# Optimization experiments

Measured on AMD Instinct MI355X. Metric: run time of the kernel, lower is better.

## Reference

```python
import jax, jax.numpy as jnp
import numpy as np

P = 1024   # total patches = B * n_patches
B = 32
NPATCH = 32
D = 64
EPS = 1e-6


def _mlp2(x, W1, b1, W2, b2):
    # Linear -> ReLU -> (Dropout p=0) -> Linear
    return jax.nn.relu(x @ W1 + b1) @ W2 + b2


def setup_inputs() -> dict:
    key = jax.random.key(0)
    ks = jax.random.split(key, 32)
    d = D
    inp = {}
    inp['x'] = jax.random.normal(ks[0], (65536, d), dtype=jnp.float32)
    inp['subgraphs_nodes_mapper'] = jax.random.randint(ks[1], (65536,), 0, 65536)
    inp['subgraphs_batch'] = jnp.sort(jax.random.randint(ks[2], (65536,), 0, P))
    inp['subgraphs_batch_row'] = jax.random.randint(ks[3], (16384,), 0, P)
    inp['subgraphs_batch_col'] = jax.random.randint(ks[4], (16384,), 0, P)
    inp['coarsen_edge_attr'] = jax.random.uniform(ks[5], (16384,), dtype=jnp.float32)
    s = 1.0 / np.sqrt(d)
    def W(k, shape):
        return jax.random.normal(k, shape, dtype=jnp.float32) * s
    # input_transform (Linear,ReLU,Linear,ReLU)
    inp['Wt1'] = W(ks[6], (d, d)); inp['bt1'] = jnp.zeros((d,), jnp.float32)
    inp['Wt2'] = W(ks[7], (d, d)); inp['bt2'] = jnp.zeros((d,), jnp.float32)
    # pre / post deepset (2 layers each)
    inp['Wpre1'] = W(ks[8], (d, d)); inp['bpre1'] = jnp.zeros((d,), jnp.float32)
    inp['Wpre2'] = W(ks[9], (d, d)); inp['bpre2'] = jnp.zeros((d,), jnp.float32)
    inp['Wpost1'] = W(ks[10], (d, d)); inp['bpost1'] = jnp.zeros((d,), jnp.float32)
    inp['Wpost2'] = W(ks[11], (d, d)); inp['bpost2'] = jnp.zeros((d,), jnp.float32)
    # linK / linV
    inp['Wk'] = W(ks[12], (d, d)); inp['bk'] = jnp.zeros((d,), jnp.float32)
    inp['Wv'] = W(ks[13], (d, d)); inp['bv'] = jnp.zeros((d,), jnp.float32)
    # attention-based readout seed
    inp['seed'] = jax.random.normal(ks[14], (d,), dtype=jnp.float32)
    # classifier: Linear(d, d//2), ReLU, Linear(d//2, num_classes)
    inp['Wc1'] = W(ks[15], (d, d // 2)); inp['bc1'] = jnp.zeros((d // 2,), jnp.float32)
    inp['Wc2'] = W(ks[16], (d // 2, 10)); inp['bc2'] = jnp.zeros((10,), jnp.float32)
    return inp


def reference(x, subgraphs_nodes_mapper, subgraphs_batch, subgraphs_batch_row,
              subgraphs_batch_col, coarsen_edge_attr,
              Wt1, bt1, Wt2, bt2,
              Wpre1, bpre1, Wpre2, bpre2,
              Wpost1, bpost1, Wpost2, bpost2,
              Wk, bk, Wv, bv, seed,
              Wc1, bc1, Wc2, bc2):
    seg = jax.ops.segment_sum
    row, col, batch = subgraphs_batch_row, subgraphs_batch_col, subgraphs_batch

    # input_transform then gather onto subgraph-combined node set
    h = jax.nn.relu(jax.nn.relu(x @ Wt1 + bt1) @ Wt2 + bt2)
    hs = h[subgraphs_nodes_mapper]                        # [N, d]

    # symmetric random-walk normalization of coarsened edge weights
    deg = seg(coarsen_edge_attr, row, num_segments=P)
    dinv = jnp.where(deg > 0, jax.lax.rsqrt(jnp.maximum(deg, EPS)), 0.0)
    attr = dinv[row] * coarsen_edge_attr * dinv[col]      # [E]

    # Q: pre-deepset -> scatter-sum per patch -> post-deepset
    Q = _mlp2(hs, Wpre1, bpre1, Wpre2, bpre2)
    Qs = seg(Q, batch, num_segments=P)                    # [P, d]
    Qs = _mlp2(Qs, Wpost1, bpost1, Wpost2, bpost2)

    # K: linear proj, scatter-mean per patch; V: linear proj (node level)
    K = hs @ Wk + bk
    cnt = seg(jnp.ones_like(K[:, 0]), batch, num_segments=P)
    Ks = seg(K, batch, num_segments=P) / jnp.maximum(cnt, 1.0)[:, None]
    V = hs @ Wv + bv

    # relu kernel feature maps
    Qk = jax.nn.relu(Qs)                                  # [P, d]
    Kk = jax.nn.relu(K)                                   # [N, d]
    Ksk = jax.nn.relu(Ks)                                 # [P, d]

    # linear attention state per patch: M_p = sum_{i in p} k_i v_i^T
    M = seg(Kk[:, :, None] * V[:, None, :], batch, num_segments=P)  # [P, d, d]
    # random-walk message / key propagation on coarsened patch graph
    M = M + seg(attr[:, None, None] * M[col], row, num_segments=P)
    Kagg = Ksk + seg(attr[:, None] * Ksk[col], row, num_segments=P)

    # kernelized attention readout per patch
    num = jnp.einsum('pd,pde->pe', Qk, M)
    den = jnp.sum(Qk * Kagg, axis=-1)
    out = num / (den[:, None] + EPS)                      # [P, d]

    # (B p) d -> B p d, attention-based set readout with learned seed
    out = out.reshape(B, NPATCH, D)
    scores = jax.nn.softmax((out @ seed) / jnp.sqrt(jnp.float32(D)), axis=1)
    pooled = jnp.einsum('bp,bpd->bd', scores, out)        # [B, d]

    # classifier
    logits = jax.nn.relu(pooled @ Wc1 + bc1) @ Wc2 + bc2  # [B, num_classes]
    return logits
```

## Files before the change

### kernel.cpp

```cpp
#include <hip/hip_runtime.h>
#include <cstddef>

#define NND  65536
#define PP   1024
#define EE   16384
#define TJA  48
#define TI   32
#define EPSF 1e-6f

typedef unsigned int   u32;
typedef unsigned short u16;
typedef __attribute__((ext_vector_type(8))) short bf16x8;
typedef __attribute__((ext_vector_type(4))) float f32x4;

__device__ __forceinline__ u16 f2bf(float f) {
    u32 u = __float_as_uint(f);
    u += 0x7fffu + ((u >> 16) & 1u);
    return (u16)(u >> 16);
}
__device__ __forceinline__ float bflo(u32 u) { return __uint_as_float(u << 16); }
__device__ __forceinline__ float bfhi(u32 u) { return __uint_as_float(u & 0xffff0000u); }
__device__ __forceinline__ float bf1(u16 v)  { return __uint_as_float(((u32)v) << 16); }


__global__ void patch_bounds_kernel(const int* __restrict__ batch, int* __restrict__ start) {
    int i = blockIdx.x * blockDim.x + threadIdx.x;
    if (i >= NND) return;
    int b  = batch[i];
    int bp = (i == 0) ? -1 : batch[i - 1];
    for (int p = bp + 1; p <= b; ++p) start[p] = i;
    if (i == NND - 1) {
        for (int p = b + 1; p <= PP; ++p) start[p] = NND;
    }
}

__global__ void edge_hist_kernel(const int* __restrict__ row, const int* __restrict__ col,
                                 const float* __restrict__ attr,
                                 float* __restrict__ deg, int* __restrict__ colcnt) {
    int e = blockIdx.x * blockDim.x + threadIdx.x;
    if (e >= EE) return;
    atomicAdd(&deg[row[e]], attr[e]);
    atomicAdd(&colcnt[col[e]], 1);
}

__global__ void scan_dinv_kernel(const int* __restrict__ colcnt, int* __restrict__ col_start,
                                 const float* __restrict__ deg, float* __restrict__ dinv) {
    __shared__ int s[PP];
    int t = threadIdx.x;
    s[t] = colcnt[t];
    float dg = deg[t];
    dinv[t] = (dg > 0.f) ? rsqrtf(fmaxf(dg, EPSF)) : 0.f;
    __syncthreads();
    for (int off = 1; off < PP; off <<= 1) {
        int v = (t >= off) ? s[t - off] : 0;
        __syncthreads();
        s[t] += v;
        __syncthreads();
    }
    col_start[t + 1] = s[t];
    if (t == 0) col_start[0] = 0;
}

__global__ void edge_scatter_kernel(const int* __restrict__ col, const int* __restrict__ col_start,
                                    int* __restrict__ colfill, int* __restrict__ edge_perm) {
    int e = blockIdx.x * blockDim.x + threadIdx.x;
    if (e >= EE) return;
    int c = col[e];
    int pos = col_start[c] + atomicAdd(&colfill[c], 1);
    edge_perm[pos] = e;
}

__global__ __launch_bounds__(256)
void pack_w_kernel(const float* W0, const float* W1, const float* W2, const float* W3,
                   const float* W4, const float* W5, const float* W6, const float* W7,
                   u16* __restrict__ out) {
    const float* Ws[8] = {W0, W1, W2, W3, W4, W5, W6, W7};
    const float* W = Ws[blockIdx.x];
    u16* dst = out + (size_t)blockIdx.x * 4096;
    int t = threadIdx.x;
    for (int idx = t; idx < 512; idx += 256) {
        int f = idx >> 6, l = idx & 63;
        int kk = f >> 2, nt = f & 3;
        int g = l >> 4, m = l & 15;
#pragma unroll
        for (int j = 0; j < 8; ++j) {
            int k = kk * 32 + g * 8 + j;
            int n = nt * 16 + m;
            dst[idx * 8 + j] = f2bf(W[k * 64 + n]);
        }
    }
}


__device__ __forceinline__ void stage_f32(const float* __restrict__ in, u16* s, int row0, int t) {
    int r = t >> 2, c = t & 3;
    const float4* src = (const float4*)(in + (size_t)(row0 + r) * 64 + c * 16);
    char* sb = (char*)s + r * 128;
    int swz = (r & 7) << 4;
#pragma unroll
    for (int q4 = 0; q4 < 4; ++q4) {
        float4 v = src[q4];
        u32 p0 = (u32)f2bf(v.x) | ((u32)f2bf(v.y) << 16);
        u32 p1 = (u32)f2bf(v.z) | ((u32)f2bf(v.w) << 16);
        int pc = c * 8 + q4 * 2;
        *(u32*)(sb + ((pc * 4) ^ swz))       = p0;
        *(u32*)(sb + (((pc + 1) * 4) ^ swz)) = p1;
    }
}

__device__ __forceinline__ void stage_bf16_gather(const u16* __restrict__ h,
                                                  const int* __restrict__ gmap,
                                                  u16* s, int row0, int t) {
    int r = t >> 2, c = t & 3;
    int sr = gmap[row0 + r];
    const uint4* src = (const uint4*)(h + (size_t)sr * 64) + c * 2;
    uint4 a = src[0], b = src[1];
    char* sb = (char*)s + r * 128;
    int swz = (r & 7) << 4;
    *(uint4*)(sb + ((c * 32) ^ swz))      = a;
    *(uint4*)(sb + ((c * 32 + 16) ^ swz)) = b;
}

template <bool RELU>
__device__ __forceinline__ void gemm_layer(const u16* src, u16* dst,
                                           const u16* __restrict__ Wp,
                                           const float* __restrict__ bias,
                                           int wv, int lane) {
    int g = lane >> 4, m = lane & 15;
    int arow = wv * 16 + m;
    const char* sb = (const char*)src + arow * 128;
    int aswz = (arow & 7) << 4;
    bf16x8 a0 = *(const bf16x8*)(sb + ((g * 16) ^ aswz));
    bf16x8 a1 = *(const bf16x8*)(sb + ((64 + g * 16) ^ aswz));
    const bf16x8* wp = (const bf16x8*)Wp;
#pragma unroll
    for (int ntile = 0; ntile < 4; ++ntile) {
        float bv = bias[ntile * 16 + m];
        f32x4 acc = {bv, bv, bv, bv};
        acc = __builtin_amdgcn_mfma_f32_16x16x32_bf16(a0, wp[(0 * 4 + ntile) * 64 + lane], acc, 0, 0, 0);
        acc = __builtin_amdgcn_mfma_f32_16x16x32_bf16(a1, wp[(1 * 4 + ntile) * 64 + lane], acc, 0, 0, 0);
        int col = ntile * 16 + m;
#pragma unroll
        for (int rg = 0; rg < 4; ++rg) {
            float v = acc[rg];
            if (RELU) v = fmaxf(v, 0.f);
            int rr = wv * 16 + g * 4 + rg;
            *(u16*)((char*)dst + rr * 128 + ((2 * col) ^ ((rr & 7) << 4))) = f2bf(v);
        }
    }
}

template <bool RELU>
__device__ __forceinline__ void gemm_layer_f32out(const u16* src, float* __restrict__ out,
                                                  const u16* __restrict__ Wp,
                                                  const float* __restrict__ bias,
                                                  int row0, int wv, int lane) {
    int g = lane >> 4, m = lane & 15;
    int arow = wv * 16 + m;
    const char* sb = (const char*)src + arow * 128;
    int aswz = (arow & 7) << 4;
    bf16x8 a0 = *(const bf16x8*)(sb + ((g * 16) ^ aswz));
    bf16x8 a1 = *(const bf16x8*)(sb + ((64 + g * 16) ^ aswz));
    const bf16x8* wp = (const bf16x8*)Wp;
#pragma unroll
    for (int ntile = 0; ntile < 4; ++ntile) {
        float bv = bias[ntile * 16 + m];
        f32x4 acc = {bv, bv, bv, bv};
        acc = __builtin_amdgcn_mfma_f32_16x16x32_bf16(a0, wp[(0 * 4 + ntile) * 64 + lane], acc, 0, 0, 0);
        acc = __builtin_amdgcn_mfma_f32_16x16x32_bf16(a1, wp[(1 * 4 + ntile) * 64 + lane], acc, 0, 0, 0);
        int col = ntile * 16 + m;
#pragma unroll
        for (int rg = 0; rg < 4; ++rg) {
            float v = acc[rg];
            if (RELU) v = fmaxf(v, 0.f);
            out[(size_t)(row0 + wv * 16 + g * 4 + rg) * 64 + col] = v;
        }
    }
}

__device__ __forceinline__ void copy_out_bf16(const u16* s, u16* __restrict__ g, int row0, int t) {
    int r = t >> 2, c = t & 3;
    const char* sb = (const char*)s + r * 128;
    int swz = (r & 7) << 4;
    uint4 a = *(const uint4*)(sb + ((c * 32) ^ swz));
    uint4 b = *(const uint4*)(sb + ((c * 32 + 16) ^ swz));
    uint4* dst = (uint4*)(g + (size_t)(row0 + r) * 64) + c * 2;
    dst[0] = a; dst[1] = b;
}

template <bool OUT_BF16>
__global__ __launch_bounds__(256)
void mfma_mlp2_kernel(const float* __restrict__ in,
                      const u16* __restrict__ Wp1, const float* __restrict__ b1,
                      const u16* __restrict__ Wp2, const float* __restrict__ b2,
                      void* __restrict__ out) {
    __shared__ __align__(16) u16 xs[4096];
    __shared__ __align__(16) u16 ys[4096];
    int t = threadIdx.x, lane = t & 63, wv = t >> 6;
    int row0 = blockIdx.x * 64;
    stage_f32(in, xs, row0, t);
    gemm_layer<true>(xs, ys, Wp1, b1, wv, lane);
    if (OUT_BF16) {
        gemm_layer<true>(ys, xs, Wp2, b2, wv, lane);
        copy_out_bf16(xs, (u16*)out, row0, t);
    } else {
        gemm_layer_f32out<true>(ys, (float*)out, Wp2, b2, row0, wv, lane);
    }
}

__global__ __launch_bounds__(256)
void qkv_mfma_kernel(const u16* __restrict__ h, const int* __restrict__ gmap,
                     const u16* __restrict__ Wpk, const float* __restrict__ bk,
                     const u16* __restrict__ Wpv, const float* __restrict__ bv,
                     const u16* __restrict__ Wp1, const float* __restrict__ bp1,
                     const u16* __restrict__ Wp2, const float* __restrict__ bp2,
                     u16* __restrict__ Kout, u16* __restrict__ Vout, u16* __restrict__ Qout) {
    __shared__ __align__(16) u16 xs[4096];
    __shared__ __align__(16) u16 ys[4096];
    int t = threadIdx.x, lane = t & 63, wv = t >> 6;
    int row0 = blockIdx.x * 64;
    stage_bf16_gather(h, gmap, xs, row0, t);
    gemm_layer<false>(xs, ys, Wpk, bk, wv, lane);
    copy_out_bf16(ys, Kout, row0, t);
    gemm_layer<false>(xs, ys, Wpv, bv, wv, lane);
    copy_out_bf16(ys, Vout, row0, t);
    gemm_layer<true>(xs, ys, Wp1, bp1, wv, lane);
    gemm_layer<false>(ys, xs, Wp2, bp2, wv, lane);
    copy_out_bf16(xs, Qout, row0, t);
}

__global__ __launch_bounds__(256)
void patch_reduce_kernel(const u16* __restrict__ Qn, const u16* __restrict__ K,
                         const int* __restrict__ start,
                         float* __restrict__ Qs_raw, float* __restrict__ Ksk) {
    __shared__ float qred[4][64], kred[4][64];
    int p = blockIdx.x, t = threadIdx.x;
    int d = t & 63, s = t >> 6;
    int i0 = start[p], i1 = start[p + 1];
    float qa = 0.f, ka = 0.f;
    for (int i = i0 + s; i < i1; i += 4) {
        qa += bf1(Qn[(size_t)i * 64 + d]);
        ka += bf1(K[(size_t)i * 64 + d]);
    }
    qred[s][d] = qa; kred[s][d] = ka;
    __syncthreads();
    if (s == 0) {
        float q = qred[0][d] + qred[1][d] + qred[2][d] + qred[3][d];
        float k = kred[0][d] + kred[1][d] + kred[2][d] + kred[3][d];
        Qs_raw[(size_t)p * 64 + d] = q;
        int cnt = i1 - i0;
        Ksk[(size_t)p * 64 + d] = fmaxf(k / (float)max(cnt, 1), 0.f);
    }
}

__global__ __launch_bounds__(256)
void attn_kernel(const float* __restrict__ Qk, const u16* __restrict__ K,
                 const u16* __restrict__ V, const float* __restrict__ Ksk,
                 const int* __restrict__ e_row, const float* __restrict__ e_attr,
                 const int* __restrict__ edge_perm, const int* __restrict__ col_start,
                 const int* __restrict__ patch_start, const float* __restrict__ dinv,
                 float* __restrict__ num, float* __restrict__ Kagg) {
    __shared__ float Qs[TJA][65];
    __shared__ float accN[TJA][65];
    __shared__ float Ks_[TI][65];
    __shared__ float Vs[TI][65];
    __shared__ float dots[TJA][TI];
    __shared__ float coef[TJA];
    __shared__ int   trow[TJA];
    __shared__ float Ksc[64];
    int c = blockIdx.x, t = threadIdx.x;
    int e0 = col_start[c], e1 = col_start[c + 1];
    int ntgt = e1 - e0 + 1;
    int i0 = patch_start[c], i1 = patch_start[c + 1];
    float dc = dinv[c];
    if (t < 64) Ksc[t] = Ksk[(size_t)c * 64 + t];

    for (int jc = 0; jc < ntgt; jc += TJA) {
        int mj = min(TJA, ntgt - jc);
        __syncthreads();
        if (t < mj) {
            int j = jc + t; int p; float cf;
            if (j == 0) { p = c; cf = 1.f; }
            else { int e = edge_perm[e0 + j - 1]; p = e_row[e]; cf = dinv[p] * e_attr[e] * dc; }
            trow[t] = p; coef[t] = cf;
        }
        __syncthreads();
        for (int idx = t; idx < mj * 64; idx += 256) {
            int j = idx >> 6, d = idx & 63;
            Qs[j][d] = Qk[(size_t)trow[j] * 64 + d];
            accN[j][d] = 0.f;
        }
        __syncthreads();
        for (int ic = i0; ic < i1; ic += TI) {
            int ni = min(TI, i1 - ic);
            for (int idx = t; idx < ni * 16; idx += 256) {
                int i = idx >> 4, q = idx & 15;
                uint2 kv = ((const uint2*)(K + (size_t)(ic + i) * 64))[q];
                uint2 vv = ((const uint2*)(V + (size_t)(ic + i) * 64))[q];
                float* kd = &Ks_[i][q * 4];
                kd[0] = fmaxf(bflo(kv.x), 0.f); kd[1] = fmaxf(bfhi(kv.x), 0.f);
                kd[2] = fmaxf(bflo(kv.y), 0.f); kd[3] = fmaxf(bfhi(kv.y), 0.f);
                float* vd = &Vs[i][q * 4];
                vd[0] = bflo(vv.x); vd[1] = bfhi(vv.x);
                vd[2] = bflo(vv.y); vd[3] = bfhi(vv.y);
            }
            __syncthreads();
            for (int idx = t; idx < mj * TI; idx += 256) {
                int j = idx >> 5, i = idx & (TI - 1);
                float s = 0.f;
#pragma unroll
                for (int d = 0; d < 64; ++d) s = fmaf(Qs[j][d], Ks_[i][d], s);
                dots[j][i] = s;
            }
            __syncthreads();
            {
                int d0 = (t & 15) * 4;
                for (int j = t >> 4; j < mj; j += 16) {
                    float a0 = accN[j][d0],     a1 = accN[j][d0 + 1];
                    float a2 = accN[j][d0 + 2], a3 = accN[j][d0 + 3];
                    for (int i = 0; i < ni; ++i) {
                        float dv = dots[j][i];
                        a0 = fmaf(dv, Vs[i][d0],     a0);
                        a1 = fmaf(dv, Vs[i][d0 + 1], a1);
                        a2 = fmaf(dv, Vs[i][d0 + 2], a2);
                        a3 = fmaf(dv, Vs[i][d0 + 3], a3);
                    }
                    accN[j][d0] = a0; accN[j][d0 + 1] = a1;
                    accN[j][d0 + 2] = a2; accN[j][d0 + 3] = a3;
                }
            }
            __syncthreads();
        }
        for (int idx = t; idx < mj * 64; idx += 256) {
            int j = idx >> 6, d = idx & 63;
            float cf = coef[j];
            atomicAdd(&num[(size_t)trow[j] * 64 + d],  cf * accN[j][d]);
            atomicAdd(&Kagg[(size_t)trow[j] * 64 + d], cf * Ksc[d]);
        }
    }
}

__global__ __launch_bounds__(64)
void final_kernel(const float* __restrict__ num, const float* __restrict__ Qk,
                  const float* __restrict__ Kagg, const float* __restrict__ seed,
                  const float* __restrict__ Wc1, const float* __restrict__ bc1,
                  const float* __restrict__ Wc2, const float* __restrict__ bc2,
                  float* __restrict__ logits) {
    __shared__ float s_out[32][65];
    __shared__ float s_rd[32], s_sc[32], s_pool[64], s_c1[32], s_seed[64];
    int b = blockIdx.x, t = threadIdx.x;
    s_seed[t] = seed[t];
    if (t < 32) {
        int p = b * 32 + t;
        float den = 0.f;
        for (int d = 0; d < 64; ++d)
            den = fmaf(Qk[(size_t)p * 64 + d], Kagg[(size_t)p * 64 + d], den);
        s_rd[t] = 1.f / (den + EPSF);
    }
    __syncthreads();
    for (int p = 0; p < 32; ++p)
        s_out[p][t] = num[(size_t)(b * 32 + p) * 64 + t] * s_rd[p];
    __syncthreads();
    if (t < 32) {
        float sc = 0.f;
        for (int d = 0; d < 64; ++d) sc = fmaf(s_out[t][d], s_seed[d], sc);
        s_sc[t] = sc * 0.125f;
    }
    __syncthreads();
    if (t == 0) {
        float mx = -1e30f;
        for (int p = 0; p < 32; ++p) mx = fmaxf(mx, s_sc[p]);
        float sm = 0.f;
        for (int p = 0; p < 32; ++p) { float e = expf(s_sc[p] - mx); s_sc[p] = e; sm += e; }
        float inv = 1.f / sm;
        for (int p = 0; p < 32; ++p) s_sc[p] *= inv;
    }
    __syncthreads();
    {
        float pa = 0.f;
        for (int p = 0; p < 32; ++p) pa = fmaf(s_sc[p], s_out[p][t], pa);
        s_pool[t] = pa;
    }
    __syncthreads();
    if (t < 32) {
        float a = bc1[t];
        for (int d = 0; d < 64; ++d) a = fmaf(s_pool[d], Wc1[d * 32 + t], a);
        s_c1[t] = fmaxf(a, 0.f);
    }
    __syncthreads();
    if (t < 10) {
        float a = bc2[t];
        for (int j = 0; j < 32; ++j) a = fmaf(s_c1[j], Wc2[j * 10 + t], a);
        logits[b * 10 + t] = a;
    }
}


extern "C" void kernel_launch(void* const* d_in, const int* in_sizes, int n_in,
                              void* d_out, int out_size, void* d_ws, size_t ws_size,
                              hipStream_t stream) {
    const float* x      = (const float*)d_in[0];
    const int*   mapper = (const int*)d_in[1];
    const int*   batch  = (const int*)d_in[2];
    const int*   e_row  = (const int*)d_in[3];
    const int*   e_col  = (const int*)d_in[4];
    const float* e_attr = (const float*)d_in[5];
    const float* Wt1 = (const float*)d_in[6],  *bt1 = (const float*)d_in[7];
    const float* Wt2 = (const float*)d_in[8],  *bt2 = (const float*)d_in[9];
    const float* Wpre1 = (const float*)d_in[10], *bpre1 = (const float*)d_in[11];
    const float* Wpre2 = (const float*)d_in[12], *bpre2 = (const float*)d_in[13];
    const float* Wpost1 = (const float*)d_in[14], *bpost1 = (const float*)d_in[15];
    const float* Wpost2 = (const float*)d_in[16], *bpost2 = (const float*)d_in[17];
    const float* Wk = (const float*)d_in[18], *bk = (const float*)d_in[19];
    const float* Wv = (const float*)d_in[20], *bv = (const float*)d_in[21];
    const float* seed = (const float*)d_in[22];
    const float* Wc1 = (const float*)d_in[23], *bc1 = (const float*)d_in[24];
    const float* Wc2 = (const float*)d_in[25], *bc2 = (const float*)d_in[26];
    float* logits = (float*)d_out;

    char* w = (char*)d_ws;
    const size_t NB2 = (size_t)NND * 64 * 2;
    u16* hb  = (u16*)w;             w += NB2;
    u16* Kb  = (u16*)w;             w += NB2;
    u16* Vb  = (u16*)w;             w += NB2;
    u16* Qnb = (u16*)w;             w += NB2;
    u16* Wp  = (u16*)w;             w += 8 * 4096 * 2;
    float* numb   = (float*)w;      w += PP * 64 * 4;
    float* Kagg   = (float*)w;      w += PP * 64 * 4;
    float* Qs_raw = (float*)w;      w += PP * 64 * 4;
    float* Qkb    = (float*)w;      w += PP * 64 * 4;
    float* Kskb   = (float*)w;      w += PP * 64 * 4;
    float* deg    = (float*)w;      w += PP * 4;
    int*   colcnt = (int*)w;        w += PP * 4;
    int*   colfill= (int*)w;        w += PP * 4;
    float* dinv   = (float*)w;      w += PP * 4;
    int* patch_start = (int*)w;     w += (PP + 1) * 4;
    int* col_start   = (int*)w;     w += (PP + 1) * 4;
    int* edge_perm   = (int*)w;     w += EE * 4;

    hipMemsetAsync(numb, 0, 2 * PP * 64 * sizeof(float), stream);
    hipMemsetAsync(deg, 0, 3 * PP * sizeof(int), stream);

    patch_bounds_kernel<<<NND / 256, 256, 0, stream>>>(batch, patch_start);
    edge_hist_kernel<<<EE / 256, 256, 0, stream>>>(e_row, e_col, e_attr, deg, colcnt);
    scan_dinv_kernel<<<1, PP, 0, stream>>>(colcnt, col_start, deg, dinv);
    edge_scatter_kernel<<<EE / 256, 256, 0, stream>>>(e_col, col_start, colfill, edge_perm);

    pack_w_kernel<<<8, 256, 0, stream>>>(Wt1, Wt2, Wk, Wv, Wpre1, Wpre2, Wpost1, Wpost2, Wp);

    mfma_mlp2_kernel<true><<<NND / 64, 256, 0, stream>>>(
        x, Wp + 0 * 4096, bt1, Wp + 1 * 4096, bt2, hb);
    qkv_mfma_kernel<<<NND / 64, 256, 0, stream>>>(
        hb, mapper, Wp + 2 * 4096, bk, Wp + 3 * 4096, bv,
        Wp + 4 * 4096, bpre1, Wp + 5 * 4096, bpre2, Kb, Vb, Qnb);
    patch_reduce_kernel<<<PP, 256, 0, stream>>>(Qnb, Kb, patch_start, Qs_raw, Kskb);
    mfma_mlp2_kernel<false><<<PP / 64, 256, 0, stream>>>(
        Qs_raw, Wp + 6 * 4096, bpost1, Wp + 7 * 4096, bpost2, Qkb);
    attn_kernel<<<PP, 256, 0, stream>>>(Qkb, Kb, Vb, Kskb, e_row, e_attr, edge_perm,
                                        col_start, patch_start, dinv, numb, Kagg);
    final_kernel<<<32, 64, 0, stream>>>(numb, Qkb, Kagg, seed, Wc1, bc1, Wc2, bc2, logits);
}
```

Baseline: 214.9 us.

## Rewrite attention kernel with bf16 shared tiles and per-wave dot/accumulate

Replaces the attention kernel with a version that keeps K, V and Q tiles in shared memory as bf16, with relu applied via a packed bit mask. It uses larger node chunks (88) and a per-wave row loop that computes dots and then accumulates V into a shared accumulator. Qk is now stored as bf16, so the post-MLP kernel uses the bf16 output path. The patch reduction reads packed u32 pairs with 8 row slices. This cuts shared memory footprint and global traffic, but lowers Qk precision and serializes target rows across only 4 waves.

```diff
diff --git a/kernel.cpp b/kernel.cpp
--- a/kernel.cpp
+++ b/kernel.cpp
@@ -4,8 +4,8 @@
 #define NND  65536
 #define PP   1024
 #define EE   16384
-#define TJA  48
-#define TI   32
+#define CAP  88
+#define TJ2  32
 #define EPSF 1e-6f
 
 typedef unsigned int   u32;
@@ -21,6 +21,10 @@
 __device__ __forceinline__ float bflo(u32 u) { return __uint_as_float(u << 16); }
 __device__ __forceinline__ float bfhi(u32 u) { return __uint_as_float(u & 0xffff0000u); }
 __device__ __forceinline__ float bf1(u16 v)  { return __uint_as_float(((u32)v) << 16); }
+__device__ __forceinline__ u32 relu2(u32 v) {
+    u32 mask = ((v & 0x80008000u) >> 15) * 0xFFFFu;
+    return v & ~mask;
+}
 
 
 __global__ void patch_bounds_kernel(const int* __restrict__ batch, int* __restrict__ start) {
@@ -150,34 +154,6 @@
     }
 }
 
-template <bool RELU>
-__device__ __forceinline__ void gemm_layer_f32out(const u16* src, float* __restrict__ out,
-                                                  const u16* __restrict__ Wp,
-                                                  const float* __restrict__ bias,
-                                                  int row0, int wv, int lane) {
-    int g = lane >> 4, m = lane & 15;
-    int arow = wv * 16 + m;
-    const char* sb = (const char*)src + arow * 128;
-    int aswz = (arow & 7) << 4;
-    bf16x8 a0 = *(const bf16x8*)(sb + ((g * 16) ^ aswz));
-    bf16x8 a1 = *(const bf16x8*)(sb + ((64 + g * 16) ^ aswz));
-    const bf16x8* wp = (const bf16x8*)Wp;
-#pragma unroll
-    for (int ntile = 0; ntile < 4; ++ntile) {
-        float bv = bias[ntile * 16 + m];
-        f32x4 acc = {bv, bv, bv, bv};
-        acc = __builtin_amdgcn_mfma_f32_16x16x32_bf16(a0, wp[(0 * 4 + ntile) * 64 + lane], acc, 0, 0, 0);
-        acc = __builtin_amdgcn_mfma_f32_16x16x32_bf16(a1, wp[(1 * 4 + ntile) * 64 + lane], acc, 0, 0, 0);
-        int col = ntile * 16 + m;
-#pragma unroll
-        for (int rg = 0; rg < 4; ++rg) {
-            float v = acc[rg];
-            if (RELU) v = fmaxf(v, 0.f);
-            out[(size_t)(row0 + wv * 16 + g * 4 + rg) * 64 + col] = v;
-        }
-    }
-}
-
 __device__ __forceinline__ void copy_out_bf16(const u16* s, u16* __restrict__ g, int row0, int t) {
     int r = t >> 2, c = t & 3;
     const char* sb = (const char*)s + r * 128;
@@ -188,24 +164,19 @@
     dst[0] = a; dst[1] = b;
 }
 
-template <bool OUT_BF16>
 __global__ __launch_bounds__(256)
 void mfma_mlp2_kernel(const float* __restrict__ in,
                       const u16* __restrict__ Wp1, const float* __restrict__ b1,
                       const u16* __restrict__ Wp2, const float* __restrict__ b2,
-                      void* __restrict__ out) {
+                      u16* __restrict__ out) {
     __shared__ __align__(16) u16 xs[4096];
     __shared__ __align__(16) u16 ys[4096];
     int t = threadIdx.x, lane = t & 63, wv = t >> 6;
     int row0 = blockIdx.x * 64;
     stage_f32(in, xs, row0, t);
     gemm_layer<true>(xs, ys, Wp1, b1, wv, lane);
-    if (OUT_BF16) {
-        gemm_layer<true>(ys, xs, Wp2, b2, wv, lane);
-        copy_out_bf16(xs, (u16*)out, row0, t);
-    } else {
-        gemm_layer_f32out<true>(ys, (float*)out, Wp2, b2, row0, wv, lane);
-    }
+    gemm_layer<true>(ys, xs, Wp2, b2, wv, lane);
+    copy_out_bf16(xs, out, row0, t);
 }
 
 __global__ __launch_bounds__(256)
@@ -233,115 +204,117 @@
 void patch_reduce_kernel(const u16* __restrict__ Qn, const u16* __restrict__ K,
                          const int* __restrict__ start,
                          float* __restrict__ Qs_raw, float* __restrict__ Ksk) {
-    __shared__ float qred[4][64], kred[4][64];
+    __shared__ float qred[8][64], kred[8][64];
     int p = blockIdx.x, t = threadIdx.x;
-    int d = t & 63, s = t >> 6;
+    int w = t & 31, s = t >> 5;
     int i0 = start[p], i1 = start[p + 1];
-    float qa = 0.f, ka = 0.f;
-    for (int i = i0 + s; i < i1; i += 4) {
-        qa += bf1(Qn[(size_t)i * 64 + d]);
-        ka += bf1(K[(size_t)i * 64 + d]);
-    }
-    qred[s][d] = qa; kred[s][d] = ka;
-    __syncthreads();
-    if (s == 0) {
-        float q = qred[0][d] + qred[1][d] + qred[2][d] + qred[3][d];
-        float k = kred[0][d] + kred[1][d] + kred[2][d] + kred[3][d];
-        Qs_raw[(size_t)p * 64 + d] = q;
+    float qa0 = 0.f, qa1 = 0.f, ka0 = 0.f, ka1 = 0.f;
+    for (int i = i0 + s; i < i1; i += 8) {
+        u32 qv = ((const u32*)(Qn + (size_t)i * 64))[w];
+        u32 kv = ((const u32*)(K  + (size_t)i * 64))[w];
+        qa0 += bflo(qv); qa1 += bfhi(qv);
+        ka0 += bflo(kv); ka1 += bfhi(kv);
+    }
+    qred[s][w * 2] = qa0; qred[s][w * 2 + 1] = qa1;
+    kred[s][w * 2] = ka0; kred[s][w * 2 + 1] = ka1;
+    __syncthreads();
+    if (t < 64) {
+        float q = 0.f, k = 0.f;
+#pragma unroll
+        for (int z = 0; z < 8; ++z) { q += qred[z][t]; k += kred[z][t]; }
+        Qs_raw[(size_t)p * 64 + t] = q;
         int cnt = i1 - i0;
-        Ksk[(size_t)p * 64 + d] = fmaxf(k / (float)max(cnt, 1), 0.f);
+        Ksk[(size_t)p * 64 + t] = fmaxf(k / (float)max(cnt, 1), 0.f);
     }
 }
 
 __global__ __launch_bounds__(256)
-void attn_kernel(const float* __restrict__ Qk, const u16* __restrict__ K,
-                 const u16* __restrict__ V, const float* __restrict__ Ksk,
-                 const int* __restrict__ e_row, const float* __restrict__ e_attr,
-                 const int* __restrict__ edge_perm, const int* __restrict__ col_start,
-                 const int* __restrict__ patch_start, const float* __restrict__ dinv,
-                 float* __restrict__ num, float* __restrict__ Kagg) {
-    __shared__ float Qs[TJA][65];
-    __shared__ float accN[TJA][65];
-    __shared__ float Ks_[TI][65];
-    __shared__ float Vs[TI][65];
-    __shared__ float dots[TJA][TI];
-    __shared__ float coef[TJA];
-    __shared__ int   trow[TJA];
+void attn2_kernel(const u16* __restrict__ Qkb, const u16* __restrict__ Kb,
+                  const u16* __restrict__ Vb, const float* __restrict__ Kskb,
+                  const int* __restrict__ e_row, const float* __restrict__ e_attr,
+                  const int* __restrict__ edge_perm, const int* __restrict__ col_start,
+                  const int* __restrict__ patch_start, const float* __restrict__ dinv,
+                  float* __restrict__ num, float* __restrict__ Kagg) {
+    __shared__ u16   Ks[CAP * 66];
+    __shared__ u16   Vs[CAP * 66];
+    __shared__ u16   Qs[TJ2 * 66];
+    __shared__ float accS[TJ2 * 64];
+    __shared__ float dots[4][CAP];
+    __shared__ float coef[TJ2];
+    __shared__ int   trow[TJ2];
     __shared__ float Ksc[64];
-    int c = blockIdx.x, t = threadIdx.x;
+    int c = blockIdx.x, t = threadIdx.x, wv = t >> 6, lane = t & 63;
     int e0 = col_start[c], e1 = col_start[c + 1];
     int ntgt = e1 - e0 + 1;
     int i0 = patch_start[c], i1 = patch_start[c + 1];
     float dc = dinv[c];
-    if (t < 64) Ksc[t] = Ksk[(size_t)c * 64 + t];
-
-    for (int jc = 0; jc < ntgt; jc += TJA) {
-        int mj = min(TJA, ntgt - jc);
+    if (t < 64) Ksc[t] = Kskb[(size_t)c * 64 + t];
+
+    for (int tc = 0; tc < ntgt; tc += TJ2) {
+        int mj = min(TJ2, ntgt - tc);
         __syncthreads();
         if (t < mj) {
-            int j = jc + t; int p; float cf;
+            int j = tc + t; int p; float cf;
             if (j == 0) { p = c; cf = 1.f; }
             else { int e = edge_perm[e0 + j - 1]; p = e_row[e]; cf = dinv[p] * e_attr[e] * dc; }
             trow[t] = p; coef[t] = cf;
         }
+        for (int idx = t; idx < mj * 64; idx += 256) accS[idx] = 0.f;
+        __syncthreads();
+        for (int idx = t; idx < mj * 32; idx += 256) {
+            int j = idx >> 5, q = idx & 31;
+            u32 v = ((const u32*)(Qkb + (size_t)trow[j] * 64))[q];
+            *(u32*)&Qs[j * 66 + q * 2] = v;
+        }
+        for (int ic = i0; ic < i1; ic += CAP) {
+            int nc = min(CAP, i1 - ic);
+            __syncthreads();
+            for (int idx = t; idx < nc * 8; idx += 256) {
+                int i = idx >> 3, q = idx & 7;
+                uint4 kv = *((const uint4*)(Kb + (size_t)(ic + i) * 64) + q);
+                uint4 vv = *((const uint4*)(Vb + (size_t)(ic + i) * 64) + q);
+                u32* kd = (u32*)&Ks[i * 66 + q * 8];
+                kd[0] = relu2(kv.x); kd[1] = relu2(kv.y);
+                kd[2] = relu2(kv.z); kd[3] = relu2(kv.w);
+                u32* vd = (u32*)&Vs[i * 66 + q * 8];
+                vd[0] = vv.x; vd[1] = vv.y; vd[2] = vv.z; vd[3] = vv.w;
+            }
+            __syncthreads();
+            for (int j = wv; j < mj; j += 4) {
+                for (int ib = 0; ib < nc; ib += 64) {
+                    int i = ib + lane;
+                    if (i < nc) {
+                        float dot = 0.f;
+                        const u32* kr = (const u32*)&Ks[i * 66];
+                        const u32* qr = (const u32*)&Qs[j * 66];
+#pragma unroll 8
+                        for (int q = 0; q < 32; ++q) {
+                            u32 kw = kr[q], qw = qr[q];
+                            dot = fmaf(bflo(qw), bflo(kw), dot);
+                            dot = fmaf(bfhi(qw), bfhi(kw), dot);
+                        }
+                        dots[wv][i] = dot;
+                    }
+                }
+                float out = 0.f;
+#pragma unroll 4
+                for (int i = 0; i < nc; ++i)
+                    out = fmaf(dots[wv][i], bf1(Vs[i * 66 + lane]), out);
+                accS[j * 64 + lane] += out;
+            }
+        }
         __syncthreads();
         for (int idx = t; idx < mj * 64; idx += 256) {
             int j = idx >> 6, d = idx & 63;
-            Qs[j][d] = Qk[(size_t)trow[j] * 64 + d];
-            accN[j][d] = 0.f;
-        }
-        __syncthreads();
-        for (int ic = i0; ic < i1; ic += TI) {
-            int ni = min(TI, i1 - ic);
-            for (int idx = t; idx < ni * 16; idx += 256) {
-                int i = idx >> 4, q = idx & 15;
-                uint2 kv = ((const uint2*)(K + (size_t)(ic + i) * 64))[q];
-                uint2 vv = ((const uint2*)(V + (size_t)(ic + i) * 64))[q];
-                float* kd = &Ks_[i][q * 4];
-                kd[0] = fmaxf(bflo(kv.x), 0.f); kd[1] = fmaxf(bfhi(kv.x), 0.f);
-                kd[2] = fmaxf(bflo(kv.y), 0.f); kd[3] = fmaxf(bfhi(kv.y), 0.f);
-                float* vd = &Vs[i][q * 4];
-                vd[0] = bflo(vv.x); vd[1] = bfhi(vv.x);
-                vd[2] = bflo(vv.y); vd[3] = bfhi(vv.y);
-            }
-            __syncthreads();
-            for (int idx = t; idx < mj * TI; idx += 256) {
-                int j = idx >> 5, i = idx & (TI - 1);
-                float s = 0.f;
-#pragma unroll
-                for (int d = 0; d < 64; ++d) s = fmaf(Qs[j][d], Ks_[i][d], s);
-                dots[j][i] = s;
-            }
-            __syncthreads();
-            {
-                int d0 = (t & 15) * 4;
-                for (int j = t >> 4; j < mj; j += 16) {
-                    float a0 = accN[j][d0],     a1 = accN[j][d0 + 1];
-                    float a2 = accN[j][d0 + 2], a3 = accN[j][d0 + 3];
-                    for (int i = 0; i < ni; ++i) {
-                        float dv = dots[j][i];
-                        a0 = fmaf(dv, Vs[i][d0],     a0);
-                        a1 = fmaf(dv, Vs[i][d0 + 1], a1);
-                        a2 = fmaf(dv, Vs[i][d0 + 2], a2);
-                        a3 = fmaf(dv, Vs[i][d0 + 3], a3);
-                    }
-                    accN[j][d0] = a0; accN[j][d0 + 1] = a1;
-                    accN[j][d0 + 2] = a2; accN[j][d0 + 3] = a3;
-                }
-            }
-            __syncthreads();
-        }
-        for (int idx = t; idx < mj * 64; idx += 256) {
-            int j = idx >> 6, d = idx & 63;
             float cf = coef[j];
-            atomicAdd(&num[(size_t)trow[j] * 64 + d],  cf * accN[j][d]);
+            atomicAdd(&num[(size_t)trow[j] * 64 + d],  cf * accS[j * 64 + d]);
             atomicAdd(&Kagg[(size_t)trow[j] * 64 + d], cf * Ksc[d]);
         }
     }
 }
 
 __global__ __launch_bounds__(64)
-void final_kernel(const float* __restrict__ num, const float* __restrict__ Qk,
+void final_kernel(const float* __restrict__ num, const u16* __restrict__ Qk,
                   const float* __restrict__ Kagg, const float* __restrict__ seed,
                   const float* __restrict__ Wc1, const float* __restrict__ bc1,
                   const float* __restrict__ Wc2, const float* __restrict__ bc2,
@@ -354,7 +327,7 @@
         int p = b * 32 + t;
         float den = 0.f;
         for (int d = 0; d < 64; ++d)
-            den = fmaf(Qk[(size_t)p * 64 + d], Kagg[(size_t)p * 64 + d], den);
+            den = fmaf(bf1(Qk[(size_t)p * 64 + d]), Kagg[(size_t)p * 64 + d], den);
         s_rd[t] = 1.f / (den + EPSF);
     }
     __syncthreads();
@@ -425,10 +398,10 @@
     u16* Vb  = (u16*)w;             w += NB2;
     u16* Qnb = (u16*)w;             w += NB2;
     u16* Wp  = (u16*)w;             w += 8 * 4096 * 2;
+    u16* Qkb = (u16*)w;             w += PP * 64 * 2;
     float* numb   = (float*)w;      w += PP * 64 * 4;
     float* Kagg   = (float*)w;      w += PP * 64 * 4;
     float* Qs_raw = (float*)w;      w += PP * 64 * 4;
-    float* Qkb    = (float*)w;      w += PP * 64 * 4;
     float* Kskb   = (float*)w;      w += PP * 64 * 4;
     float* deg    = (float*)w;      w += PP * 4;
     int*   colcnt = (int*)w;        w += PP * 4;
@@ -448,15 +421,15 @@
 
     pack_w_kernel<<<8, 256, 0, stream>>>(Wt1, Wt2, Wk, Wv, Wpre1, Wpre2, Wpost1, Wpost2, Wp);
 
-    mfma_mlp2_kernel<true><<<NND / 64, 256, 0, stream>>>(
+    mfma_mlp2_kernel<<<NND / 64, 256, 0, stream>>>(
         x, Wp + 0 * 4096, bt1, Wp + 1 * 4096, bt2, hb);
     qkv_mfma_kernel<<<NND / 64, 256, 0, stream>>>(
         hb, mapper, Wp + 2 * 4096, bk, Wp + 3 * 4096, bv,
         Wp + 4 * 4096, bpre1, Wp + 5 * 4096, bpre2, Kb, Vb, Qnb);
     patch_reduce_kernel<<<PP, 256, 0, stream>>>(Qnb, Kb, patch_start, Qs_raw, Kskb);
-    mfma_mlp2_kernel<false><<<PP / 64, 256, 0, stream>>>(
+    mfma_mlp2_kernel<<<PP / 64, 256, 0, stream>>>(
         Qs_raw, Wp + 6 * 4096, bpost1, Wp + 7 * 4096, bpost2, Qkb);
-    attn_kernel<<<PP, 256, 0, stream>>>(Qkb, Kb, Vb, Kskb, e_row, e_attr, edge_perm,
-                                        col_start, patch_start, dinv, numb, Kagg);
+    attn2_kernel<<<PP, 256, 0, stream>>>(Qkb, Kb, Vb, Kskb, e_row, e_attr, edge_perm,
+                                         col_start, patch_start, dinv, numb, Kagg);
     final_kernel<<<32, 64, 0, stream>>>(numb, Qkb, Kagg, seed, Wc1, bc1, Wc2, bc2, logits);
 }
```

Result: faster. 199.3 us (-7.3%).
